# Performance work log

Hardware: AMD Instinct MI355X
Metric: run time of the kernel (lower is better)

## Reference

```python
import jax, jax.numpy as jnp
import numpy as np

N = 50000
E = 800000
IN_DIM = 128
HID = 128
HEADS = 8
OUT_DIM = 64
NEG_SLOPE = 0.2


def setup_inputs() -> dict:
    key = jax.random.key(0)
    ks = jax.random.split(key, 10)
    x = jax.random.normal(ks[0], (N, IN_DIM), dtype=jnp.float32)
    edge_index = jax.random.randint(ks[1], (2, E), 0, N, dtype=jnp.int64)
    c1 = HID // HEADS  # 16 per-head channels, layer 1
    # layer 1 params (GATConv: lin has no bias; att_src/att_dst are [1,H,C])
    W1 = jax.random.normal(ks[2], (IN_DIM, HEADS * c1), dtype=jnp.float32) * 0.1
    att_src1 = jax.random.normal(ks[3], (1, HEADS, c1), dtype=jnp.float32) * 0.1
    att_dst1 = jax.random.normal(ks[4], (1, HEADS, c1), dtype=jnp.float32) * 0.1
    b1 = jnp.zeros((HEADS * c1,), dtype=jnp.float32)  # concat=True -> bias size H*C
    # layer 2 params (heads=1, concat=False)
    W2 = jax.random.normal(ks[5], (HID, OUT_DIM), dtype=jnp.float32) * 0.1
    att_src2 = jax.random.normal(ks[6], (1, 1, OUT_DIM), dtype=jnp.float32) * 0.1
    att_dst2 = jax.random.normal(ks[7], (1, 1, OUT_DIM), dtype=jnp.float32) * 0.1
    b2 = jnp.zeros((OUT_DIM,), dtype=jnp.float32)
    return {"x": x, "edge_index": edge_index,
            "W1": W1, "att_src1": att_src1, "att_dst1": att_dst1, "b1": b1,
            "W2": W2, "att_src2": att_src2, "att_dst2": att_dst2, "b2": b2}


def _gat_conv(x, src, dst, W, att_src, att_dst, bias, heads, concat):
    n = x.shape[0]
    c = W.shape[1] // heads
    h = (x @ W).reshape(n, heads, c)                      # [N,H,C]
    a_src = jnp.sum(h * att_src, axis=-1)                 # [N,H]
    a_dst = jnp.sum(h * att_dst, axis=-1)                 # [N,H]
    e = a_src[src] + a_dst[dst]                           # [E,H]
    e = jnp.where(e > 0, e, NEG_SLOPE * e)                # leaky_relu
    # segment softmax over incoming edges of each dst node
    m = jax.ops.segment_max(e, dst, num_segments=n)       # [N,H]
    ex = jnp.exp(e - m[dst])
    denom = jax.ops.segment_sum(ex, dst, num_segments=n)  # [N,H]
    alpha = ex / (denom[dst] + 1e-16)                     # [E,H]
    msg = h[src] * alpha[:, :, None]                      # [E,H,C]
    out = jax.ops.segment_sum(msg, dst, num_segments=n)   # [N,H,C]
    out = out.reshape(n, heads * c) if concat else out.mean(axis=1)
    return out + bias


def reference(x, edge_index, W1, att_src1, att_dst1, b1, W2, att_src2, att_dst2, b2):
    # add self-loops (PyG GATConv default add_self_loops=True)
    loops = jnp.arange(N, dtype=edge_index.dtype)
    src = jnp.concatenate([edge_index[0], loops])
    dst = jnp.concatenate([edge_index[1], loops])
    h = _gat_conv(x, src, dst, W1, att_src1, att_dst1, b1, HEADS, True)
    h = jax.nn.elu(h)
    out = _gat_conv(h, src, dst, W2, att_src2, att_dst2, b2, 1, False)
    return jax.nn.log_softmax(out, axis=1)
```

## Files before the change

### kernel.cpp

```cpp
#include <hip/hip_runtime.h>
#include <math.h>

#define N_NODES 50000
#define E_EDGES 800000
#define ET      (E_EDGES + N_NODES)
#define IN_DIM  128
#define HID     128
#define HEADS   8
#define C1      16
#define OUT_DIM 64
#define NEG_SLOPE 0.2f
#define LOG2E   1.4426950408889634f

#define TILE    8192
#define NT      ((ET + TILE - 1) / TILE)
#define NB      ((N_NODES + 255) / 256)

#define CONV_BLOCKS (N_NODES * IN_DIM / 4 / 256)
#define PREP_BLOCKS 112
#define MEGA_A (NT + CONV_BLOCKS + PREP_BLOCKS)
#define L1T_BLOCKS ((N_NODES + 63) / 64)
#define MEGA_B (NB + L1T_BLOCKS)

typedef unsigned int uint32;
typedef __attribute__((ext_vector_type(8))) short bf16x8;
typedef __attribute__((ext_vector_type(4))) float f32x4;

static __device__ __forceinline__ unsigned short f2bf(float f) {
    uint32 u = __float_as_uint(f);
    u += 0x7FFFu + ((u >> 16) & 1u);
    return (unsigned short)(u >> 16);
}


__global__ __launch_bounds__(256) void prep_all(
        const int* __restrict__ dst, int* __restrict__ cnt,
        const float* __restrict__ x, unsigned short* __restrict__ xb,
        const float* __restrict__ W1, const float* __restrict__ as1,
        const float* __restrict__ ad1, const float* __restrict__ W2,
        const float* __restrict__ as2, const float* __restrict__ ad2,
        unsigned short* __restrict__ w1t, unsigned short* __restrict__ p1t,
        unsigned short* __restrict__ w2t, unsigned short* __restrict__ p2t) {
    __shared__ int hist[NB];
    int blk = blockIdx.x, t = threadIdx.x;
    if (blk < NT) {
        for (int b = t; b < NB; b += 256) hist[b] = 0;
        __syncthreads();
        int base = blk * TILE;
        #pragma unroll
        for (int it = 0; it < TILE / 256; ++it) {
            int i = base + it * 256 + t;
            if (i < ET) {
                int d = (i < E_EDGES) ? dst[i] : (i - E_EDGES);
                atomicAdd(&hist[d >> 8], 1);
            }
        }
        __syncthreads();
        for (int b = t; b < NB; b += 256) cnt[blk * NB + b] = hist[b];
    } else if (blk < NT + CONV_BLOCKS) {
        int i = (blk - NT) * 256 + t;
        float4 v = ((const float4*)x)[i];
        ushort4 o;
        o.x = f2bf(v.x); o.y = f2bf(v.y); o.z = f2bf(v.z); o.w = f2bf(v.w);
        ((ushort4*)xb)[i] = o;
    } else {
        int b = blk - NT - CONV_BLOCKS;
        if (b < 64) {
            int i = b * 256 + t;
            int n = i >> 7, k = i & 127;
            w1t[n * IN_DIM + k] = f2bf(W1[k * HID + n]);
        } else if (b < 96) {
            int i = (b - 64) * 256 + t;
            int n = i >> 7, k = i & 127;
            w2t[n * HID + k] = f2bf(W2[k * OUT_DIM + n]);
        } else if (b < 104) {
            int i = (b - 96) * 256 + t;
            int j = i >> 7, k = i & 127;
            int hh = j & 7;
            const float* a = (j < 8) ? as1 : ad1;
            float acc = 0.f;
            #pragma unroll
            for (int c = 0; c < C1; ++c)
                acc = fmaf(W1[k * HID + hh * C1 + c], a[hh * C1 + c], acc);
            p1t[j * IN_DIM + k] = f2bf(acc * LOG2E);
        } else {
            int i = (b - 104) * 256 + t;
            int j = i >> 7, k = i & 127;
            if (j < 2) {
                const float* a = (j == 0) ? as2 : ad2;
                float acc = 0.f;
                #pragma unroll
                for (int c = 0; c < OUT_DIM; ++c)
                    acc = fmaf(W2[k * OUT_DIM + c], a[c], acc);
                p2t[j * HID + k] = f2bf(acc * LOG2E);
            } else {
                p2t[j * HID + k] = 0;
            }
        }
    }
}


__global__ __launch_bounds__(256) void bucket_scatter(
        const int* __restrict__ src, const int* __restrict__ dst,
        const int* __restrict__ cnt, int* __restrict__ bucketStart,
        uint32* __restrict__ pairs) {
    __shared__ int lcur[NB];
    __shared__ int sscan[256];
    int t = threadIdx.x;
    int tile = blockIdx.x;

    int run = 0, total = 0;
    if (t < NB) {
        for (int k = 0; k < NT; ++k) {
            int c = cnt[k * NB + t];
            if (k < tile) run += c;
            total += c;
        }
    }
    sscan[t] = (t < NB) ? total : 0;
    __syncthreads();
    #pragma unroll
    for (int off = 1; off < 256; off <<= 1) {
        int add = (t >= off) ? sscan[t - off] : 0;
        __syncthreads();
        sscan[t] += add;
        __syncthreads();
    }
    int bstart = sscan[t] - total;
    if (t < NB) {
        lcur[t] = bstart + run;
        if (tile == 0) bucketStart[t] = bstart;
    }
    if (tile == 0 && t == 0) bucketStart[NB] = ET;
    __syncthreads();

    int base = tile * TILE;
    #pragma unroll
    for (int it = 0; it < TILE / 256; ++it) {
        int i = base + it * 256 + t;
        if (i < ET) {
            int s, d;
            if (i < E_EDGES) { s = src[i]; d = dst[i]; }
            else             { s = d = i - E_EDGES; }
            int pos = atomicAdd(&lcur[d >> 8], 1);
            pairs[pos] = ((uint32)s << 8) | (uint32)(d & 255);
        }
    }
}


__global__ __launch_bounds__(256) void build_l1t(
        const uint32* __restrict__ pairs, const int* __restrict__ bucketStart,
        int* __restrict__ row_start, int* __restrict__ csr_src,
        const unsigned short* __restrict__ xb, const unsigned short* __restrict__ w1t,
        const unsigned short* __restrict__ p1t, unsigned short* __restrict__ h1b,
        float* __restrict__ a_src, float* __restrict__ a_dst) {
    __shared__ int sdeg[256];
    __shared__ int sscan[256];
    int t = threadIdx.x;
    if (blockIdx.x < NB) {
        int b = blockIdx.x;
        int beg = bucketStart[b], end = bucketStart[b + 1];
        sdeg[t] = 0;
        __syncthreads();
        for (int j = beg + t; j < end; j += 256)
            atomicAdd(&sdeg[pairs[j] & 255u], 1);
        __syncthreads();
        int v = sdeg[t];
        sscan[t] = v;
        __syncthreads();
        #pragma unroll
        for (int off = 1; off < 256; off <<= 1) {
            int add = (t >= off) ? sscan[t - off] : 0;
            __syncthreads();
            sscan[t] += add;
            __syncthreads();
        }
        int pos0 = beg + sscan[t] - v;
        int n = b * 256 + t;
        if (n < N_NODES) row_start[n] = pos0;
        if (b == 0 && t == 0) row_start[N_NODES] = ET;
        __syncthreads();
        sscan[t] = pos0;
        __syncthreads();
        for (int j = beg + t; j < end; j += 256) {
            uint32 p = pairs[j];
            int pos = atomicAdd(&sscan[p & 255u], 1);
            csr_src[pos] = (int)(p >> 8);
        }
        return;
    }
    int bb = blockIdx.x - NB;
    int w = t >> 6, lane = t & 63;
    int l15 = lane & 15, quad = lane >> 4;
    int n0 = bb * 64 + w * 16;
    int mrow = n0 + l15;
    int mload = (mrow < N_NODES) ? mrow : (N_NODES - 1);

    bf16x8 af[4];
    #pragma unroll
    for (int s = 0; s < 4; ++s)
        af[s] = *(const bf16x8*)&xb[(size_t)mload * IN_DIM + s * 32 + quad * 8];

    #pragma unroll
    for (int tt = 0; tt < 9; ++tt) {
        const unsigned short* Brow = (tt < 8) ? &w1t[(tt * 16 + l15) * IN_DIM]
                                              : &p1t[l15 * IN_DIM];
        f32x4 acc = {0.f, 0.f, 0.f, 0.f};
        #pragma unroll
        for (int s = 0; s < 4; ++s) {
            bf16x8 bf = *(const bf16x8*)&Brow[s * 32 + quad * 8];
            acc = __builtin_amdgcn_mfma_f32_16x16x32_bf16(af[s], bf, acc, 0, 0, 0);
        }
        int nodeb = n0 + quad * 4;
        if (tt < 8) {
            int ch = tt * 16 + l15;
            #pragma unroll
            for (int r = 0; r < 4; ++r)
                if (nodeb + r < N_NODES)
                    h1b[(size_t)(nodeb + r) * HID + ch] = f2bf(acc[r]);
        } else {
            #pragma unroll
            for (int r = 0; r < 4; ++r) {
                if (nodeb + r < N_NODES) {
                    if (l15 < 8) a_src[(nodeb + r) * HEADS + l15] = acc[r];
                    else         a_dst[(nodeb + r) * HEADS + (l15 - 8)] = acc[r];
                }
            }
        }
    }
}


__global__ __launch_bounds__(128) void l1_aggregate(
        const unsigned short* __restrict__ h1b, const float* __restrict__ a_src,
        const float* __restrict__ a_dst, const int* __restrict__ row_start,
        const int* __restrict__ csr_src, const float* __restrict__ b1,
        unsigned short* __restrict__ h_act_b) {
    int t = threadIdx.x;
    int w = t >> 6;
    uint32 lane = t & 63;
    uint32 quarter = lane >> 4;
    uint32 lane16 = lane & 15;
    int n = blockIdx.x * 8 + w * 4 + (int)quarter;
    uint32 c0 = lane16 * 8u;
    uint32 h = lane16 >> 1;
    int beg = row_start[n], end = row_start[n + 1];
    int cnt = end - beg;
    int kmax = cnt;
    kmax = max(kmax, __shfl_xor(kmax, 16, 64));
    kmax = max(kmax, __shfl_xor(kmax, 32, 64));
    float adst = a_dst[n * HEADS + h];
    float l = 0.f;
    float a0 = 0.f, a1 = 0.f, a2 = 0.f, a3 = 0.f;
    float a4 = 0.f, a5 = 0.f, a6 = 0.f, a7 = 0.f;

    for (int k = 0; k < kmax; k += 4) {
        uint32 ss[4]; float ee[4]; uint4 uu[4];
        #pragma unroll
        for (int q = 0; q < 4; ++q) {
            int j = beg + k + q;
            int jc = (j < end) ? j : (end - 1);
            ss[q] = (uint32)csr_src[jc];
        }
        #pragma unroll
        for (int q = 0; q < 4; ++q) ee[q] = a_src[ss[q] * 8u + h];
        #pragma unroll
        for (int q = 0; q < 4; ++q) uu[q] = *(const uint4*)&h1b[(ss[q] << 7) + c0];
        #pragma unroll
        for (int q = 0; q < 4; ++q) {
            float e = ee[q] + adst;
            e = fmaxf(e, NEG_SLOPE * e);
            e = (k + q < cnt) ? e : -10000.f;
            float p = exp2f(e);
            l += p;
            a0 = fmaf(p, __uint_as_float(uu[q].x << 16), a0);
            a1 = fmaf(p, __uint_as_float(uu[q].x & 0xFFFF0000u), a1);
            a2 = fmaf(p, __uint_as_float(uu[q].y << 16), a2);
            a3 = fmaf(p, __uint_as_float(uu[q].y & 0xFFFF0000u), a3);
            a4 = fmaf(p, __uint_as_float(uu[q].z << 16), a4);
            a5 = fmaf(p, __uint_as_float(uu[q].z & 0xFFFF0000u), a5);
            a6 = fmaf(p, __uint_as_float(uu[q].w << 16), a6);
            a7 = fmaf(p, __uint_as_float(uu[q].w & 0xFFFF0000u), a7);
        }
    }

    float inv = 1.f / (l + 1e-16f);
    float v0 = a0 * inv + b1[c0 + 0];
    float v1 = a1 * inv + b1[c0 + 1];
    float v2 = a2 * inv + b1[c0 + 2];
    float v3 = a3 * inv + b1[c0 + 3];
    float v4 = a4 * inv + b1[c0 + 4];
    float v5 = a5 * inv + b1[c0 + 5];
    float v6 = a6 * inv + b1[c0 + 6];
    float v7 = a7 * inv + b1[c0 + 7];
    v0 = v0 > 0.f ? v0 : (__expf(v0) - 1.f);
    v1 = v1 > 0.f ? v1 : (__expf(v1) - 1.f);
    v2 = v2 > 0.f ? v2 : (__expf(v2) - 1.f);
    v3 = v3 > 0.f ? v3 : (__expf(v3) - 1.f);
    v4 = v4 > 0.f ? v4 : (__expf(v4) - 1.f);
    v5 = v5 > 0.f ? v5 : (__expf(v5) - 1.f);
    v6 = v6 > 0.f ? v6 : (__expf(v6) - 1.f);
    v7 = v7 > 0.f ? v7 : (__expf(v7) - 1.f);
    uint4 packed;
    packed.x = (uint32)f2bf(v0) | ((uint32)f2bf(v1) << 16);
    packed.y = (uint32)f2bf(v2) | ((uint32)f2bf(v3) << 16);
    packed.z = (uint32)f2bf(v4) | ((uint32)f2bf(v5) << 16);
    packed.w = (uint32)f2bf(v6) | ((uint32)f2bf(v7) << 16);
    *(uint4*)&h_act_b[(size_t)n * HID + c0] = packed;
}


__global__ __launch_bounds__(256) void l2_transform_mfma(
        const unsigned short* __restrict__ h_act_b, const unsigned short* __restrict__ w2t,
        const unsigned short* __restrict__ p2t, unsigned short* __restrict__ h2b,
        float* __restrict__ a_src2, float* __restrict__ a_dst2) {
    int t = threadIdx.x, w = t >> 6, lane = t & 63;
    int l15 = lane & 15, quad = lane >> 4;
    int n0 = blockIdx.x * 64 + w * 16;
    int mrow = n0 + l15;
    int mload = (mrow < N_NODES) ? mrow : (N_NODES - 1);

    bf16x8 af[4];
    #pragma unroll
    for (int s = 0; s < 4; ++s)
        af[s] = *(const bf16x8*)&h_act_b[(size_t)mload * HID + s * 32 + quad * 8];

    #pragma unroll
    for (int tt = 0; tt < 5; ++tt) {
        const unsigned short* Brow = (tt < 4) ? &w2t[(tt * 16 + l15) * HID]
                                              : &p2t[l15 * HID];
        f32x4 acc = {0.f, 0.f, 0.f, 0.f};
        #pragma unroll
        for (int s = 0; s < 4; ++s) {
            bf16x8 bf = *(const bf16x8*)&Brow[s * 32 + quad * 8];
            acc = __builtin_amdgcn_mfma_f32_16x16x32_bf16(af[s], bf, acc, 0, 0, 0);
        }
        int nodeb = n0 + quad * 4;
        if (tt < 4) {
            int ch = tt * 16 + l15;
            #pragma unroll
            for (int r = 0; r < 4; ++r)
                if (nodeb + r < N_NODES)
                    h2b[(size_t)(nodeb + r) * OUT_DIM + ch] = f2bf(acc[r]);
        } else {
            #pragma unroll
            for (int r = 0; r < 4; ++r) {
                if (nodeb + r < N_NODES) {
                    if (l15 == 0) a_src2[nodeb + r] = acc[r];
                    else if (l15 == 1) a_dst2[nodeb + r] = acc[r];
                }
            }
        }
    }
}


__global__ __launch_bounds__(128) void l2_aggregate(
        const unsigned short* __restrict__ h2b, const float* __restrict__ a_src2,
        const float* __restrict__ a_dst2, const int* __restrict__ row_start,
        const int* __restrict__ csr_src, const float* __restrict__ b2,
        float* __restrict__ out) {
    int t = threadIdx.x;
    int w = t >> 6;
    uint32 lane = t & 63;
    uint32 quarter = lane >> 4;
    uint32 lane16 = lane & 15;
    int n = blockIdx.x * 8 + w * 4 + (int)quarter;
    uint32 c0 = lane16 * 4u;
    int beg = row_start[n], end = row_start[n + 1];
    int cnt = end - beg;
    int kmax = cnt;
    kmax = max(kmax, __shfl_xor(kmax, 16, 64));
    kmax = max(kmax, __shfl_xor(kmax, 32, 64));
    float adst = a_dst2[n];
    float l = 0.f, a0 = 0.f, a1 = 0.f, a2 = 0.f, a3 = 0.f;

    for (int k = 0; k < kmax; k += 4) {
        uint32 ss[4]; float ee[4]; uint2 uu[4];
        #pragma unroll
        for (int q = 0; q < 4; ++q) {
            int j = beg + k + q;
            int jc = (j < end) ? j : (end - 1);
            ss[q] = (uint32)csr_src[jc];
        }
        #pragma unroll
        for (int q = 0; q < 4; ++q) ee[q] = a_src2[ss[q]];
        #pragma unroll
        for (int q = 0; q < 4; ++q) uu[q] = *(const uint2*)&h2b[(ss[q] << 6) + c0];
        #pragma unroll
        for (int q = 0; q < 4; ++q) {
            float e = ee[q] + adst;
            e = fmaxf(e, NEG_SLOPE * e);
            e = (k + q < cnt) ? e : -10000.f;
            float p = exp2f(e);
            l += p;
            a0 = fmaf(p, __uint_as_float(uu[q].x << 16), a0);
            a1 = fmaf(p, __uint_as_float(uu[q].x & 0xFFFF0000u), a1);
            a2 = fmaf(p, __uint_as_float(uu[q].y << 16), a2);
            a3 = fmaf(p, __uint_as_float(uu[q].y & 0xFFFF0000u), a3);
        }
    }

    float inv = 1.f / (l + 1e-16f);
    float o0 = a0 * inv + b2[c0 + 0];
    float o1 = a1 * inv + b2[c0 + 1];
    float o2 = a2 * inv + b2[c0 + 2];
    float o3 = a3 * inv + b2[c0 + 3];
    float mx = fmaxf(fmaxf(o0, o1), fmaxf(o2, o3));
    #pragma unroll
    for (int m = 8; m > 0; m >>= 1) mx = fmaxf(mx, __shfl_xor(mx, m, 16));
    float ex = __expf(o0 - mx) + __expf(o1 - mx) + __expf(o2 - mx) + __expf(o3 - mx);
    #pragma unroll
    for (int m = 8; m > 0; m >>= 1) ex += __shfl_xor(ex, m, 16);
    float lse = mx + __logf(ex);
    float4 o = make_float4(o0 - lse, o1 - lse, o2 - lse, o3 - lse);
    *(float4*)&out[(size_t)n * OUT_DIM + c0] = o;
}


extern "C" void kernel_launch(void* const* d_in, const int* in_sizes, int n_in,
                              void* d_out, int out_size, void* d_ws, size_t ws_size,
                              hipStream_t stream) {
    const float* x   = (const float*)d_in[0];
    const int*   ei  = (const int*)d_in[1];
    const float* W1  = (const float*)d_in[2];
    const float* as1 = (const float*)d_in[3];
    const float* ad1 = (const float*)d_in[4];
    const float* b1  = (const float*)d_in[5];
    const float* W2  = (const float*)d_in[6];
    const float* as2 = (const float*)d_in[7];
    const float* ad2 = (const float*)d_in[8];
    const float* b2  = (const float*)d_in[9];
    float* out = (float*)d_out;

    const int* src = ei;
    const int* dst = ei + E_EDGES;

    char* ws = (char*)d_ws;
    size_t off = 0;
    auto alloc = [&](size_t bytes) -> void* {
        void* p = ws + off;
        off += (bytes + 255) & ~size_t(255);
        return p;
    };
    unsigned short* xb     = (unsigned short*)alloc((size_t)N_NODES * IN_DIM * 2);
    unsigned short* h1b    = (unsigned short*)alloc((size_t)N_NODES * HID * 2);
    unsigned short* h_act_b= (unsigned short*)alloc((size_t)N_NODES * HID * 2);
    unsigned short* h2b    = (unsigned short*)alloc((size_t)N_NODES * OUT_DIM * 2);
    unsigned short* w1t    = (unsigned short*)alloc((size_t)HID * IN_DIM * 2);
    unsigned short* p1t    = (unsigned short*)alloc((size_t)16 * IN_DIM * 2);
    unsigned short* w2t    = (unsigned short*)alloc((size_t)OUT_DIM * HID * 2);
    unsigned short* p2t    = (unsigned short*)alloc((size_t)16 * HID * 2);
    float* a_src1    = (float*)alloc((size_t)N_NODES * HEADS * 4);
    float* a_dst1    = (float*)alloc((size_t)N_NODES * HEADS * 4);
    float* a_src2    = (float*)alloc((size_t)N_NODES * 4);
    float* a_dst2    = (float*)alloc((size_t)N_NODES * 4);
    int*   row_start = (int*)alloc((size_t)(N_NODES + 1) * 4);
    int*   csr_src   = (int*)alloc((size_t)ET * 4);
    uint32* pairs    = (uint32*)alloc((size_t)ET * 4);
    int*   cnt       = (int*)alloc((size_t)NB * NT * 4);
    int*   bucketStart = (int*)alloc((size_t)(NB + 1) * 4);

    prep_all<<<MEGA_A, 256, 0, stream>>>(dst, cnt, x, xb, W1, as1, ad1,
                                         W2, as2, ad2, w1t, p1t, w2t, p2t);
    bucket_scatter<<<NT, 256, 0, stream>>>(src, dst, cnt, bucketStart, pairs);
    build_l1t<<<MEGA_B, 256, 0, stream>>>(pairs, bucketStart, row_start, csr_src,
                                          xb, w1t, p1t, h1b, a_src1, a_dst1);
    l1_aggregate<<<N_NODES / 8, 128, 0, stream>>>(h1b, a_src1, a_dst1, row_start, csr_src, b1, h_act_b);
    l2_transform_mfma<<<L1T_BLOCKS, 256, 0, stream>>>(h_act_b, w2t, p2t, h2b, a_src2, a_dst2);
    l2_aggregate<<<N_NODES / 8, 128, 0, stream>>>(h2b, a_src2, a_dst2, row_start, csr_src, b2, out);
}
```

Baseline: 219.2 us.

## Fuse layer-1 aggregation with layer-2 MFMA transform via shared-memory tile

Merges the layer-1 aggregation kernel and the layer-2 MFMA transform into one kernel. Each 256-thread block aggregates 64 nodes in four passes and writes the bf16 activations into an XOR-swizzled LDS tile. After a barrier, the MFMA transform reads that tile. This drops one launch and the global write and re-read of the N x 128 activation buffer. In exchange each block now does four serial aggregation passes, so fewer blocks expose less parallelism for the latency-bound gathers, and the barrier stalls on the slowest node in the tile.

```diff
diff --git a/kernel.cpp b/kernel.cpp
--- a/kernel.cpp
+++ b/kernel.cpp
@@ -233,123 +233,133 @@
 }
 
 
-__global__ __launch_bounds__(128) void l1_aggregate(
+__global__ __launch_bounds__(256) void l1agg_l2t(
         const unsigned short* __restrict__ h1b, const float* __restrict__ a_src,
         const float* __restrict__ a_dst, const int* __restrict__ row_start,
         const int* __restrict__ csr_src, const float* __restrict__ b1,
-        unsigned short* __restrict__ h_act_b) {
+        const unsigned short* __restrict__ w2t, const unsigned short* __restrict__ p2t,
+        unsigned short* __restrict__ h2b, float* __restrict__ a_src2,
+        float* __restrict__ a_dst2) {
+    __shared__ unsigned short ha[64][128];
     int t = threadIdx.x;
     int w = t >> 6;
     uint32 lane = t & 63;
     uint32 quarter = lane >> 4;
     uint32 lane16 = lane & 15;
-    int n = blockIdx.x * 8 + w * 4 + (int)quarter;
-    uint32 c0 = lane16 * 8u;
-    uint32 h = lane16 >> 1;
-    int beg = row_start[n], end = row_start[n + 1];
-    int cnt = end - beg;
-    int kmax = cnt;
-    kmax = max(kmax, __shfl_xor(kmax, 16, 64));
-    kmax = max(kmax, __shfl_xor(kmax, 32, 64));
-    float adst = a_dst[n * HEADS + h];
-    float l = 0.f;
-    float a0 = 0.f, a1 = 0.f, a2 = 0.f, a3 = 0.f;
-    float a4 = 0.f, a5 = 0.f, a6 = 0.f, a7 = 0.f;
-
-    for (int k = 0; k < kmax; k += 4) {
-        uint32 ss[4]; float ee[4]; uint4 uu[4];
-        #pragma unroll
-        for (int q = 0; q < 4; ++q) {
-            int j = beg + k + q;
-            int jc = (j < end) ? j : (end - 1);
-            ss[q] = (uint32)csr_src[jc];
-        }
-        #pragma unroll
-        for (int q = 0; q < 4; ++q) ee[q] = a_src[ss[q] * 8u + h];
-        #pragma unroll
-        for (int q = 0; q < 4; ++q) uu[q] = *(const uint4*)&h1b[(ss[q] << 7) + c0];
-        #pragma unroll
-        for (int q = 0; q < 4; ++q) {
-            float e = ee[q] + adst;
-            e = fmaxf(e, NEG_SLOPE * e);
-            e = (k + q < cnt) ? e : -10000.f;
-            float p = exp2f(e);
-            l += p;
-            a0 = fmaf(p, __uint_as_float(uu[q].x << 16), a0);
-            a1 = fmaf(p, __uint_as_float(uu[q].x & 0xFFFF0000u), a1);
-            a2 = fmaf(p, __uint_as_float(uu[q].y << 16), a2);
-            a3 = fmaf(p, __uint_as_float(uu[q].y & 0xFFFF0000u), a3);
-            a4 = fmaf(p, __uint_as_float(uu[q].z << 16), a4);
-            a5 = fmaf(p, __uint_as_float(uu[q].z & 0xFFFF0000u), a5);
-            a6 = fmaf(p, __uint_as_float(uu[q].w << 16), a6);
-            a7 = fmaf(p, __uint_as_float(uu[q].w & 0xFFFF0000u), a7);
-        }
-    }
-
-    float inv = 1.f / (l + 1e-16f);
-    float v0 = a0 * inv + b1[c0 + 0];
-    float v1 = a1 * inv + b1[c0 + 1];
-    float v2 = a2 * inv + b1[c0 + 2];
-    float v3 = a3 * inv + b1[c0 + 3];
-    float v4 = a4 * inv + b1[c0 + 4];
-    float v5 = a5 * inv + b1[c0 + 5];
-    float v6 = a6 * inv + b1[c0 + 6];
-    float v7 = a7 * inv + b1[c0 + 7];
-    v0 = v0 > 0.f ? v0 : (__expf(v0) - 1.f);
-    v1 = v1 > 0.f ? v1 : (__expf(v1) - 1.f);
-    v2 = v2 > 0.f ? v2 : (__expf(v2) - 1.f);
-    v3 = v3 > 0.f ? v3 : (__expf(v3) - 1.f);
-    v4 = v4 > 0.f ? v4 : (__expf(v4) - 1.f);
-    v5 = v5 > 0.f ? v5 : (__expf(v5) - 1.f);
-    v6 = v6 > 0.f ? v6 : (__expf(v6) - 1.f);
-    v7 = v7 > 0.f ? v7 : (__expf(v7) - 1.f);
-    uint4 packed;
-    packed.x = (uint32)f2bf(v0) | ((uint32)f2bf(v1) << 16);
-    packed.y = (uint32)f2bf(v2) | ((uint32)f2bf(v3) << 16);
-    packed.z = (uint32)f2bf(v4) | ((uint32)f2bf(v5) << 16);
-    packed.w = (uint32)f2bf(v6) | ((uint32)f2bf(v7) << 16);
-    *(uint4*)&h_act_b[(size_t)n * HID + c0] = packed;
-}
-
-
-__global__ __launch_bounds__(256) void l2_transform_mfma(
-        const unsigned short* __restrict__ h_act_b, const unsigned short* __restrict__ w2t,
-        const unsigned short* __restrict__ p2t, unsigned short* __restrict__ h2b,
-        float* __restrict__ a_src2, float* __restrict__ a_dst2) {
-    int t = threadIdx.x, w = t >> 6, lane = t & 63;
-    int l15 = lane & 15, quad = lane >> 4;
-    int n0 = blockIdx.x * 64 + w * 16;
-    int mrow = n0 + l15;
-    int mload = (mrow < N_NODES) ? mrow : (N_NODES - 1);
-
-    bf16x8 af[4];
-    #pragma unroll
-    for (int s = 0; s < 4; ++s)
-        af[s] = *(const bf16x8*)&h_act_b[(size_t)mload * HID + s * 32 + quad * 8];
-
-    #pragma unroll
-    for (int tt = 0; tt < 5; ++tt) {
-        const unsigned short* Brow = (tt < 4) ? &w2t[(tt * 16 + l15) * HID]
-                                              : &p2t[l15 * HID];
-        f32x4 acc = {0.f, 0.f, 0.f, 0.f};
+    int n0blk = blockIdx.x * 64;
+
+    {
+        uint32 c0 = lane16 * 8u;
+        uint32 h = lane16 >> 1;
+        #pragma unroll
+        for (int pass = 0; pass < 4; ++pass) {
+            int n_local = w * 16 + pass * 4 + (int)quarter;
+            int n = n0blk + n_local;
+            int nc = (n < N_NODES) ? n : (N_NODES - 1);
+            int beg = row_start[nc], end = row_start[nc + 1];
+            int cnt = end - beg;
+            int kmax = cnt;
+            kmax = max(kmax, __shfl_xor(kmax, 16, 64));
+            kmax = max(kmax, __shfl_xor(kmax, 32, 64));
+            float adst = a_dst[nc * HEADS + h];
+            float l = 0.f;
+            float a0 = 0.f, a1 = 0.f, a2 = 0.f, a3 = 0.f;
+            float a4 = 0.f, a5 = 0.f, a6 = 0.f, a7 = 0.f;
+
+            for (int k = 0; k < kmax; k += 4) {
+                uint32 ss[4]; float ee[4]; uint4 uu[4];
+                #pragma unroll
+                for (int q = 0; q < 4; ++q) {
+                    int j = beg + k + q;
+                    int jc = (j < end) ? j : (end - 1);
+                    ss[q] = (uint32)csr_src[jc];
+                }
+                #pragma unroll
+                for (int q = 0; q < 4; ++q) ee[q] = a_src[ss[q] * 8u + h];
+                #pragma unroll
+                for (int q = 0; q < 4; ++q) uu[q] = *(const uint4*)&h1b[(ss[q] << 7) + c0];
+                #pragma unroll
+                for (int q = 0; q < 4; ++q) {
+                    float e = ee[q] + adst;
+                    e = fmaxf(e, NEG_SLOPE * e);
+                    e = (k + q < cnt) ? e : -10000.f;
+                    float p = exp2f(e);
+                    l += p;
+                    a0 = fmaf(p, __uint_as_float(uu[q].x << 16), a0);
+                    a1 = fmaf(p, __uint_as_float(uu[q].x & 0xFFFF0000u), a1);
+                    a2 = fmaf(p, __uint_as_float(uu[q].y << 16), a2);
+                    a3 = fmaf(p, __uint_as_float(uu[q].y & 0xFFFF0000u), a3);
+                    a4 = fmaf(p, __uint_as_float(uu[q].z << 16), a4);
+                    a5 = fmaf(p, __uint_as_float(uu[q].z & 0xFFFF0000u), a5);
+                    a6 = fmaf(p, __uint_as_float(uu[q].w << 16), a6);
+                    a7 = fmaf(p, __uint_as_float(uu[q].w & 0xFFFF0000u), a7);
+                }
+            }
+
+            float inv = 1.f / (l + 1e-16f);
+            float v0 = a0 * inv + b1[c0 + 0];
+            float v1 = a1 * inv + b1[c0 + 1];
+            float v2 = a2 * inv + b1[c0 + 2];
+            float v3 = a3 * inv + b1[c0 + 3];
+            float v4 = a4 * inv + b1[c0 + 4];
+            float v5 = a5 * inv + b1[c0 + 5];
+            float v6 = a6 * inv + b1[c0 + 6];
+            float v7 = a7 * inv + b1[c0 + 7];
+            v0 = v0 > 0.f ? v0 : (__expf(v0) - 1.f);
+            v1 = v1 > 0.f ? v1 : (__expf(v1) - 1.f);
+            v2 = v2 > 0.f ? v2 : (__expf(v2) - 1.f);
+            v3 = v3 > 0.f ? v3 : (__expf(v3) - 1.f);
+            v4 = v4 > 0.f ? v4 : (__expf(v4) - 1.f);
+            v5 = v5 > 0.f ? v5 : (__expf(v5) - 1.f);
+            v6 = v6 > 0.f ? v6 : (__expf(v6) - 1.f);
+            v7 = v7 > 0.f ? v7 : (__expf(v7) - 1.f);
+            uint4 packed;
+            packed.x = (uint32)f2bf(v0) | ((uint32)f2bf(v1) << 16);
+            packed.y = (uint32)f2bf(v2) | ((uint32)f2bf(v3) << 16);
+            packed.z = (uint32)f2bf(v4) | ((uint32)f2bf(v5) << 16);
+            packed.w = (uint32)f2bf(v6) | ((uint32)f2bf(v7) << 16);
+            uint32 g = lane16 ^ ((uint32)n_local & 15u);
+            *(uint4*)&ha[n_local][g * 8] = packed;
+        }
+    }
+    __syncthreads();
+
+    {
+        int l15 = (int)lane16, quad = (int)quarter;
+        int n0 = n0blk + w * 16;
+        int nloc = w * 16 + l15;
+
+        bf16x8 af[4];
         #pragma unroll
         for (int s = 0; s < 4; ++s) {
-            bf16x8 bf = *(const bf16x8*)&Brow[s * 32 + quad * 8];
-            acc = __builtin_amdgcn_mfma_f32_16x16x32_bf16(af[s], bf, acc, 0, 0, 0);
-        }
-        int nodeb = n0 + quad * 4;
-        if (tt < 4) {
-            int ch = tt * 16 + l15;
+            uint32 g = (uint32)(s * 4 + quad) ^ (uint32)l15;
+            af[s] = *(const bf16x8*)&ha[nloc][g * 8];
+        }
+
+        #pragma unroll
+        for (int tt = 0; tt < 5; ++tt) {
+            const unsigned short* Brow = (tt < 4) ? &w2t[(tt * 16 + l15) * HID]
+                                                  : &p2t[l15 * HID];
+            f32x4 acc = {0.f, 0.f, 0.f, 0.f};
             #pragma unroll
-            for (int r = 0; r < 4; ++r)
-                if (nodeb + r < N_NODES)
-                    h2b[(size_t)(nodeb + r) * OUT_DIM + ch] = f2bf(acc[r]);
-        } else {
-            #pragma unroll
-            for (int r = 0; r < 4; ++r) {
-                if (nodeb + r < N_NODES) {
-                    if (l15 == 0) a_src2[nodeb + r] = acc[r];
-                    else if (l15 == 1) a_dst2[nodeb + r] = acc[r];
+            for (int s = 0; s < 4; ++s) {
+                bf16x8 bf = *(const bf16x8*)&Brow[s * 32 + quad * 8];
+                acc = __builtin_amdgcn_mfma_f32_16x16x32_bf16(af[s], bf, acc, 0, 0, 0);
+            }
+            int nodeb = n0 + quad * 4;
+            if (tt < 4) {
+                int ch = tt * 16 + l15;
+                #pragma unroll
+                for (int r = 0; r < 4; ++r)
+                    if (nodeb + r < N_NODES)
+                        h2b[(size_t)(nodeb + r) * OUT_DIM + ch] = f2bf(acc[r]);
+            } else {
+                #pragma unroll
+                for (int r = 0; r < 4; ++r) {
+                    if (nodeb + r < N_NODES) {
+                        if (l15 == 0) a_src2[nodeb + r] = acc[r];
+                        else if (l15 == 1) a_dst2[nodeb + r] = acc[r];
+                    }
                 }
             }
         }
@@ -447,7 +457,6 @@
     };
     unsigned short* xb     = (unsigned short*)alloc((size_t)N_NODES * IN_DIM * 2);
     unsigned short* h1b    = (unsigned short*)alloc((size_t)N_NODES * HID * 2);
-    unsigned short* h_act_b= (unsigned short*)alloc((size_t)N_NODES * HID * 2);
     unsigned short* h2b    = (unsigned short*)alloc((size_t)N_NODES * OUT_DIM * 2);
     unsigned short* w1t    = (unsigned short*)alloc((size_t)HID * IN_DIM * 2);
     unsigned short* p1t    = (unsigned short*)alloc((size_t)16 * IN_DIM * 2);
@@ -468,7 +477,7 @@
     bucket_scatter<<<NT, 256, 0, stream>>>(src, dst, cnt, bucketStart, pairs);
     build_l1t<<<MEGA_B, 256, 0, stream>>>(pairs, bucketStart, row_start, csr_src,
                                           xb, w1t, p1t, h1b, a_src1, a_dst1);
-    l1_aggregate<<<N_NODES / 8, 128, 0, stream>>>(h1b, a_src1, a_dst1, row_start, csr_src, b1, h_act_b);
-    l2_transform_mfma<<<L1T_BLOCKS, 256, 0, stream>>>(h_act_b, w2t, p2t, h2b, a_src2, a_dst2);
+    l1agg_l2t<<<L1T_BLOCKS, 256, 0, stream>>>(h1b, a_src1, a_dst1, row_start, csr_src,
+                                              b1, w2t, p2t, h2b, a_src2, a_dst2);
     l2_aggregate<<<N_NODES / 8, 128, 0, stream>>>(h2b, a_src2, a_dst2, row_start, csr_src, b2, out);
 }
```

New measurement: 212.6 us. 3.0% less time.
